# Kernel tuning notes

Hardware: AMD Instinct MI355X
Metric: run time of the kernel (lower is better)

The kernel has to match this reference:

```python
import jax, jax.numpy as jnp
import numpy as np

N = 200000
D_IN = 512
D_OUT = 128

def _xavier(key, shape, gain=1.414):
    fan_in, fan_out = shape
    a = gain * np.sqrt(6.0 / (fan_in + fan_out))
    return jax.random.uniform(key, shape, jnp.float32, -a, a)

def setup_inputs() -> dict:
    key = jax.random.key(0)
    k0, k1, k2, k3 = jax.random.split(key, 4)
    h = jax.random.normal(k0, (N, D_IN), jnp.float32)
    W_Q = _xavier(k1, (D_IN, D_OUT))
    W_K = _xavier(k2, (D_IN, D_OUT))
    W_V = _xavier(k3, (D_IN, D_OUT))
    return {"h": h, "W_Q": W_Q, "W_K": W_K, "W_V": W_V}

def reference(h, W_Q, W_K, W_V):
    # feature maps: elu(x)+1 (positive features for linear attention)
    Q = jax.nn.elu(h @ W_Q) + 1.0          # [N, d]
    K = jax.nn.elu(h @ W_K) + 1.0          # [N, d]
    V = h @ W_V                            # [N, d]
    KV = K.T @ V                           # [d, d] summary
    k_sum = K.sum(axis=0)                  # [d]  (== K.t().sum(dim=1) row-sum per feature)
    Z = 1.0 / (Q @ k_sum[:, None])         # [N, 1]
    out = (Q @ KV) * Z                     # [N, d]
    return jax.nn.elu(out)                 # concat=True -> elu
```

## Files before the change

### kernel.cpp

```cpp
#include <hip/hip_runtime.h>
#include <stdint.h>
#include <stddef.h>


typedef __attribute__((ext_vector_type(8))) short bf16x8;
typedef __attribute__((ext_vector_type(4))) short bf16x4;
typedef __attribute__((ext_vector_type(4))) float f32x4;

#define NROWS   200000
#define DIN     512
#define DOUT    128
#define NCHUNK  3125
#define PA_BLOCKS 512

#define MFMA16(A, B, C) __builtin_amdgcn_mfma_f32_16x16x32_bf16(A, B, C, 0, 0, 0)

__device__ __forceinline__ short f2bf(float f) {
  unsigned u = __builtin_bit_cast(unsigned, f);
  u = (u + 0x7fffu + ((u >> 16) & 1u)) >> 16;
  return (short)u;
}
__device__ __forceinline__ float bf2f(short b) {
  unsigned u = ((unsigned)(unsigned short)b) << 16;
  return __builtin_bit_cast(float, u);
}

__global__ void prep_wt(const float* __restrict__ wq, const float* __restrict__ wk,
                        const float* __restrict__ wv, short* __restrict__ wt) {
  int gid = blockIdx.x * 256 + threadIdx.x;
  int k   = gid >> 5;
  int j4  = (gid & 31) * 4;
  int which = k >> 9;
  int kk    = k & 511;
  const float* W = (which == 0) ? wq : (which == 1) ? wk : wv;
  f32x4 v = *(const f32x4*)(W + (size_t)kk * DOUT + j4);
#pragma unroll
  for (int e = 0; e < 4; ++e)
    wt[(size_t)(which * DOUT + j4 + e) * DIN + kk] = f2bf(v[e]);
}

__global__ __launch_bounds__(512, 2) void pass_a(
    const float* __restrict__ h, const short* __restrict__ wt,
    short* __restrict__ q_ws, float* __restrict__ kv_part,
    float* __restrict__ ksum_part) {
  __shared__ __attribute__((aligned(16))) char smem[32768];
  const int tid = threadIdx.x;
  const int w  = tid >> 6;
  const int l  = tid & 63;
  const int lq = l >> 4;
  const int lr = l & 15;
  const int bid = blockIdx.x;

  const int arow = tid >> 3;
  const int akq  = tid & 7;
  const int sxa  = (arow ^ (arow >> 2)) & 3;
  char* const a_wptr = smem + arow * 64 +
      ((((akq >> 1) ^ sxa) & 3) << 4) + (akq & 1) * 8;

  const int sxl = (lr ^ (lr >> 2)) & 3;
  const char* const a_rbase = smem + lr * 64 + (((lq ^ sxl) & 3) << 4);
  const char* const b_rbase = smem + 4096 + lr * 64 + (((lq ^ sxl) & 3) << 4);

  int b_dst[3], b_src[3];
#pragma unroll
  for (int q = 0; q < 3; ++q) {
    int cc  = q * 512 + tid;
    int col = cc >> 2;
    int sl  = cc & 3;
    int sx  = (col ^ (col >> 2)) & 3;
    b_dst[q] = 4096 + cc * 16;
    b_src[q] = col * DIN + ((sl ^ sx) & 3) * 8;
  }

  const f32x4 zero4 = {0.f, 0.f, 0.f, 0.f};
  f32x4 kvacc[8];
#pragma unroll
  for (int jt = 0; jt < 8; ++jt) kvacc[jt] = zero4;
  float ksum_acc = 0.f;

  for (int c = bid; c < NCHUNK; c += PA_BLOCKS) {
    f32x4 accQ[4], accK[4], accV[4];
#pragma unroll
    for (int rt = 0; rt < 4; ++rt) { accQ[rt] = zero4; accK[rt] = zero4; accV[rt] = zero4; }

    const float* hrow = h + (size_t)(c * 64 + arow) * DIN + akq * 4;
    f32x4  aReg  = *(const f32x4*)(hrow);
    bf16x8 bReg0 = *(const bf16x8*)(wt + b_src[0]);
    bf16x8 bReg1 = *(const bf16x8*)(wt + b_src[1]);
    bf16x8 bReg2 = *(const bf16x8*)(wt + b_src[2]);

    for (int t = 0; t < 16; ++t) {
      __syncthreads();
      bf16x4 a4;
      a4[0] = f2bf(aReg[0]); a4[1] = f2bf(aReg[1]);
      a4[2] = f2bf(aReg[2]); a4[3] = f2bf(aReg[3]);
      *(bf16x4*)a_wptr = a4;
      *(bf16x8*)(smem + b_dst[0]) = bReg0;
      *(bf16x8*)(smem + b_dst[1]) = bReg1;
      *(bf16x8*)(smem + b_dst[2]) = bReg2;
      __syncthreads();
      if (t < 15) {
        aReg  = *(const f32x4*)(hrow + (t + 1) * 32);
        bReg0 = *(const bf16x8*)(wt + b_src[0] + (t + 1) * 32);
        bReg1 = *(const bf16x8*)(wt + b_src[1] + (t + 1) * 32);
        bReg2 = *(const bf16x8*)(wt + b_src[2] + (t + 1) * 32);
      }
      bf16x8 af[4];
#pragma unroll
      for (int rt = 0; rt < 4; ++rt)
        af[rt] = *(const bf16x8*)(a_rbase + rt * 1024);
      bf16x8 bq = *(const bf16x8*)(b_rbase + (w)      * 1024);
      bf16x8 bk = *(const bf16x8*)(b_rbase + (w + 8)  * 1024);
      bf16x8 bv = *(const bf16x8*)(b_rbase + (w + 16) * 1024);
#pragma unroll
      for (int rt = 0; rt < 4; ++rt) {
        accQ[rt] = MFMA16(af[rt], bq, accQ[rt]);
        accK[rt] = MFMA16(af[rt], bk, accK[rt]);
        accV[rt] = MFMA16(af[rt], bv, accV[rt]);
      }
    }

    const int qcol = w * 16 + lr;
    float ks = 0.f;
#pragma unroll
    for (int rt = 0; rt < 4; ++rt) {
      f32x4 qe, ke;
#pragma unroll
      for (int f = 0; f < 4; ++f) {
        float x = accQ[rt][f];
        qe[f] = (x > 0.f) ? (x + 1.f) : __expf(x);
        float y = accK[rt][f];
        ke[f] = (y > 0.f) ? (y + 1.f) : __expf(y);
      }
      short* qp = q_ws + (size_t)(c * 64 + rt * 16 + lq * 4) * DOUT + qcol;
      qp[0]        = f2bf(qe[0]);
      qp[DOUT]     = f2bf(qe[1]);
      qp[2 * DOUT] = f2bf(qe[2]);
      qp[3 * DOUT] = f2bf(qe[3]);
      ks += ke[0] + ke[1] + ke[2] + ke[3];
      bf16x4 kp, vp;
#pragma unroll
      for (int f = 0; f < 4; ++f) { kp[f] = f2bf(ke[f]); vp[f] = f2bf(accV[rt][f]); }
      const int i  = w * 16 + lr;
      const int wb = i * 128 +
          ((((rt * 2 + (lq >> 1)) ^ (lr & 7)) & 7) << 4) + (lq & 1) * 8;
      *(bf16x4*)(smem + wb)          = kp;
      *(bf16x4*)(smem + 16384 + wb)  = vp;
    }
    ks += __shfl_xor(ks, 16);
    ks += __shfl_xor(ks, 32);
    ksum_acc += ks;
    __syncthreads();
#pragma unroll
    for (int ksb = 0; ksb < 2; ++ksb) {
      const int rslot = ((ksb * 4 + lq) ^ (lr & 7)) & 7;
      bf16x8 ka = *(const bf16x8*)(smem + (w * 16 + lr) * 128 + (rslot << 4));
#pragma unroll
      for (int jt = 0; jt < 8; ++jt) {
        bf16x8 vb = *(const bf16x8*)(smem + 16384 + (jt * 16 + lr) * 128 + (rslot << 4));
        kvacc[jt] = MFMA16(ka, vb, kvacc[jt]);
      }
    }
    __syncthreads();
  }

  float* kvp = kv_part + (size_t)bid * 16384;
#pragma unroll
  for (int jt = 0; jt < 8; ++jt)
#pragma unroll
    for (int f = 0; f < 4; ++f)
      kvp[(w * 16 + lq * 4 + f) * 128 + jt * 16 + lr] = kvacc[jt][f];
  if (lq == 0) ksum_part[bid * 128 + w * 16 + lr] = ksum_acc;
}

__global__ void reduce_kv(const float* __restrict__ kv_part,
                          const float* __restrict__ ksum_part,
                          short* __restrict__ kvT, float* __restrict__ ksum) {
  if (blockIdx.x < 128) {
    const int i  = blockIdx.x;
    const int t  = threadIdx.x;
    const int j4 = t & 31;
    const int bs = t >> 5;
    f32x4 acc = {0.f, 0.f, 0.f, 0.f};
#pragma unroll 4
    for (int b = bs * 128; b < bs * 128 + 128; ++b)
      acc += *(const f32x4*)(kv_part + (size_t)b * 16384 + i * 128 + j4 * 4);
    __shared__ f32x4 red[4][32];
    red[bs][j4] = acc;
    __syncthreads();
    if (t < 32) {
      f32x4 s = red[0][t] + red[1][t] + red[2][t] + red[3][t];
#pragma unroll
      for (int e = 0; e < 4; ++e) {
        int j = t * 4 + e;
        kvT[j * 128 + (i ^ ((j & 7) << 3))] = f2bf(s[e]);
      }
    }
  } else {
    const int j = threadIdx.x;
    float s = 0.f;
#pragma unroll 8
    for (int b = 0; b < PA_BLOCKS; ++b) s += ksum_part[b * 128 + j];
    ksum[j] = s;
  }
}

__global__ __launch_bounds__(256, 4) void pass_c(
    const short* __restrict__ q_ws, const short* __restrict__ kvT,
    const float* __restrict__ ksum, float* __restrict__ out) {
  __shared__ __attribute__((aligned(16))) char smem[33024];
  const int tid = threadIdx.x;
  const int w  = tid >> 6, l = tid & 63, lq = l >> 4, lr = l & 15;
  const int rowbase = blockIdx.x * 64 + w * 16;

#pragma unroll
  for (int q = 0; q < 8; ++q) {
    int cc = q * 256 + tid;
    *(bf16x8*)(smem + cc * 16) = *(const bf16x8*)(kvT + cc * 8);
  }

  bf16x8 qa[4];
  float d = 0.f;
  const short* qrow = q_ws + (size_t)(rowbase + lr) * DOUT + lq * 8;
#pragma unroll
  for (int ks = 0; ks < 4; ++ks) {
    qa[ks] = *(const bf16x8*)(qrow + ks * 32);
    f32x4 k0 = *(const f32x4*)(ksum + ks * 32 + lq * 8);
    f32x4 k1 = *(const f32x4*)(ksum + ks * 32 + lq * 8 + 4);
#pragma unroll
    for (int e = 0; e < 4; ++e) d += bf2f(qa[ks][e]) * k0[e];
#pragma unroll
    for (int e = 0; e < 4; ++e) d += bf2f(qa[ks][e + 4]) * k1[e];
  }
  d += __shfl_xor(d, 16);
  d += __shfl_xor(d, 32);
  float* dlds = (float*)(smem + 32768);
  if (l < 16) dlds[w * 16 + lr] = d;
  __syncthreads();

  const f32x4 zero4 = {0.f, 0.f, 0.f, 0.f};
  f32x4 acc[8];
#pragma unroll
  for (int jt = 0; jt < 8; ++jt) acc[jt] = zero4;
#pragma unroll
  for (int ks = 0; ks < 4; ++ks) {
#pragma unroll
    for (int jt = 0; jt < 8; ++jt) {
      const int j    = jt * 16 + lr;
      const int slot = (ks * 4 + lq) ^ (lr & 7);
      bf16x8 bv = *(const bf16x8*)(smem + j * 256 + (slot << 4));
      acc[jt] = MFMA16(qa[ks], bv, acc[jt]);
    }
  }
  float z[4];
#pragma unroll
  for (int f = 0; f < 4; ++f) z[f] = 1.f / dlds[w * 16 + lq * 4 + f];
#pragma unroll
  for (int jt = 0; jt < 8; ++jt) {
#pragma unroll
    for (int f = 0; f < 4; ++f) {
      float v = acc[jt][f] * z[f];
      v = (v > 0.f) ? v : (__expf(v) - 1.f);
      out[(size_t)(rowbase + lq * 4 + f) * DOUT + jt * 16 + lr] = v;
    }
  }
}

extern "C" void kernel_launch(void* const* d_in, const int* in_sizes, int n_in,
                              void* d_out, int out_size, void* d_ws, size_t ws_size,
                              hipStream_t stream) {
  const float* h  = (const float*)d_in[0];
  const float* wq = (const float*)d_in[1];
  const float* wk = (const float*)d_in[2];
  const float* wv = (const float*)d_in[3];
  char* ws = (char*)d_ws;
  short* q_ws      = (short*)(ws);
  short* wt        = (short*)(ws + 51200000);
  float* kv_part   = (float*)(ws + 51593216);
  float* ksum_part = (float*)(ws + 85147648);
  short* kvT       = (short*)(ws + 85409792);
  float* ksum      = (float*)(ws + 85442560);
  float* out       = (float*)d_out;

  prep_wt<<<dim3(192), dim3(256), 0, stream>>>(wq, wk, wv, wt);
  pass_a<<<dim3(PA_BLOCKS), dim3(512), 0, stream>>>(h, wt, q_ws, kv_part, ksum_part);
  reduce_kv<<<dim3(129), dim3(128), 0, stream>>>(kv_part, ksum_part, kvT, ksum);
  pass_c<<<dim3(NCHUNK), dim3(256), 0, stream>>>(q_ws, kvT, ksum, out);
}
```

Before: 838.9 us.

## Split projection into per-weight LDS-resident GEMM tiles with separate KV reduction pass

```diff
diff --git a/kernel.cpp b/kernel.cpp
--- a/kernel.cpp
+++ b/kernel.cpp
@@ -4,14 +4,11 @@
 
 
 typedef __attribute__((ext_vector_type(8))) short bf16x8;
-typedef __attribute__((ext_vector_type(4))) short bf16x4;
 typedef __attribute__((ext_vector_type(4))) float f32x4;
 
 #define NROWS   200000
 #define DIN     512
 #define DOUT    128
-#define NCHUNK  3125
-#define PA_BLOCKS 512
 
 #define MFMA16(A, B, C) __builtin_amdgcn_mfma_f32_16x16x32_bf16(A, B, C, 0, 0, 0)
 
@@ -28,180 +25,203 @@
 __global__ void prep_wt(const float* __restrict__ wq, const float* __restrict__ wk,
                         const float* __restrict__ wv, short* __restrict__ wt) {
   int gid = blockIdx.x * 256 + threadIdx.x;
-  int k   = gid >> 5;
-  int j4  = (gid & 31) * 4;
-  int which = k >> 9;
-  int kk    = k & 511;
-  const float* W = (which == 0) ? wq : (which == 1) ? wk : wv;
-  f32x4 v = *(const f32x4*)(W + (size_t)kk * DOUT + j4);
-#pragma unroll
-  for (int e = 0; e < 4; ++e)
-    wt[(size_t)(which * DOUT + j4 + e) * DIN + kk] = f2bf(v[e]);
-}
-
-__global__ __launch_bounds__(512, 2) void pass_a(
+  int z   = gid >> 13;
+  int col = (gid >> 6) & 127;
+  int s   = gid & 63;
+  const float* W = (z == 0) ? wq : (z == 1) ? wk : wv;
+  bf16x8 o;
+#pragma unroll
+  for (int e = 0; e < 8; ++e)
+    o[e] = f2bf(W[(size_t)(s * 8 + e) * DOUT + col]);
+  *(bf16x8*)((char*)wt + (size_t)z * 131072 + col * 1024 + ((s ^ (col & 7)) * 16)) = o;
+}
+
+__global__ __launch_bounds__(512) void pass_a(
     const float* __restrict__ h, const short* __restrict__ wt,
-    short* __restrict__ q_ws, float* __restrict__ kv_part,
-    float* __restrict__ ksum_part) {
-  __shared__ __attribute__((aligned(16))) char smem[32768];
+    short* __restrict__ q_ws, short* __restrict__ k_ws, short* __restrict__ v_ws) {
+  extern __shared__ __attribute__((aligned(16))) char smem[];
+
+  const int bid  = blockIdx.x;
+  const int xcd  = bid & 7;
+  const int slot = bid >> 3;
+  const int nT   = (xcd < 6) ? 98 : 97;
+  if ((slot / 3) >= nT) return;
+  const int base = (xcd < 6) ? xcd * 98 : 6 * 98 + (xcd - 6) * 97;
+  const int tile = base + slot / 3;
+  const int z    = slot % 3;
+
   const int tid = threadIdx.x;
-  const int w  = tid >> 6;
-  const int l  = tid & 63;
-  const int lq = l >> 4;
-  const int lr = l & 15;
-  const int bid = blockIdx.x;
-
-  const int arow = tid >> 3;
-  const int akq  = tid & 7;
-  const int sxa  = (arow ^ (arow >> 2)) & 3;
-  char* const a_wptr = smem + arow * 64 +
-      ((((akq >> 1) ^ sxa) & 3) << 4) + (akq & 1) * 8;
-
-  const int sxl = (lr ^ (lr >> 2)) & 3;
-  const char* const a_rbase = smem + lr * 64 + (((lq ^ sxl) & 3) << 4);
-  const char* const b_rbase = smem + 4096 + lr * 64 + (((lq ^ sxl) & 3) << 4);
-
-  int b_dst[3], b_src[3];
-#pragma unroll
-  for (int q = 0; q < 3; ++q) {
-    int cc  = q * 512 + tid;
-    int col = cc >> 2;
-    int sl  = cc & 3;
-    int sx  = (col ^ (col >> 2)) & 3;
-    b_dst[q] = 4096 + cc * 16;
-    b_src[q] = col * DIN + ((sl ^ sx) & 3) * 8;
-  }
-
-  const f32x4 zero4 = {0.f, 0.f, 0.f, 0.f};
-  f32x4 kvacc[8];
-#pragma unroll
-  for (int jt = 0; jt < 8; ++jt) kvacc[jt] = zero4;
-  float ksum_acc = 0.f;
-
-  for (int c = bid; c < NCHUNK; c += PA_BLOCKS) {
-    f32x4 accQ[4], accK[4], accV[4];
-#pragma unroll
-    for (int rt = 0; rt < 4; ++rt) { accQ[rt] = zero4; accK[rt] = zero4; accV[rt] = zero4; }
-
-    const float* hrow = h + (size_t)(c * 64 + arow) * DIN + akq * 4;
-    f32x4  aReg  = *(const f32x4*)(hrow);
-    bf16x8 bReg0 = *(const bf16x8*)(wt + b_src[0]);
-    bf16x8 bReg1 = *(const bf16x8*)(wt + b_src[1]);
-    bf16x8 bReg2 = *(const bf16x8*)(wt + b_src[2]);
-
-    for (int t = 0; t < 16; ++t) {
-      __syncthreads();
-      bf16x4 a4;
-      a4[0] = f2bf(aReg[0]); a4[1] = f2bf(aReg[1]);
-      a4[2] = f2bf(aReg[2]); a4[3] = f2bf(aReg[3]);
-      *(bf16x4*)a_wptr = a4;
-      *(bf16x8*)(smem + b_dst[0]) = bReg0;
-      *(bf16x8*)(smem + b_dst[1]) = bReg1;
-      *(bf16x8*)(smem + b_dst[2]) = bReg2;
-      __syncthreads();
-      if (t < 15) {
-        aReg  = *(const f32x4*)(hrow + (t + 1) * 32);
-        bReg0 = *(const bf16x8*)(wt + b_src[0] + (t + 1) * 32);
-        bReg1 = *(const bf16x8*)(wt + b_src[1] + (t + 1) * 32);
-        bReg2 = *(const bf16x8*)(wt + b_src[2] + (t + 1) * 32);
+  const int wv  = tid >> 6;
+  const int l   = tid & 63;
+  const int lr  = l & 15;
+  const int lq  = l >> 4;
+
+  {
+    const char* src = (const char*)wt + (size_t)z * 131072;
+    typedef const __attribute__((address_space(1))) char glb_c;
+    typedef __attribute__((address_space(3))) char lds_c;
+#pragma unroll
+    for (int r = 0; r < 16; ++r) {
+      int off = r * 8192 + (wv * 64) * 16;
+      __builtin_amdgcn_global_load_lds((glb_c*)(src + off + l * 16),
+                                       (lds_c*)(smem + off), 16, 0, 0);
+    }
+  }
+  __syncthreads();
+
+  size_t row0 = (size_t)tile * 256 + wv * 32 + lr;
+  size_t row1 = row0 + 16;
+  size_t r0c = (row0 < NROWS) ? row0 : (size_t)(NROWS - 1);
+  size_t r1c = (row1 < NROWS) ? row1 : (size_t)(NROWS - 1);
+  const float* a0p = h + r0c * DIN + lq * 8;
+  const float* a1p = h + r1c * DIN + lq * 8;
+
+  f32x4 acc[2][8];
+#pragma unroll
+  for (int rt = 0; rt < 2; ++rt)
+#pragma unroll
+    for (int ct = 0; ct < 8; ++ct) acc[rt][ct] = (f32x4){0.f, 0.f, 0.f, 0.f};
+
+  f32x4 c00 = *(const f32x4*)(a0p),     c01 = *(const f32x4*)(a0p + 4);
+  f32x4 c10 = *(const f32x4*)(a1p),     c11 = *(const f32x4*)(a1p + 4);
+
+  for (int ks = 0; ks < 16; ++ks) {
+    f32x4 n00, n01, n10, n11;
+    if (ks < 15) {
+      n00 = *(const f32x4*)(a0p + (ks + 1) * 32);
+      n01 = *(const f32x4*)(a0p + (ks + 1) * 32 + 4);
+      n10 = *(const f32x4*)(a1p + (ks + 1) * 32);
+      n11 = *(const f32x4*)(a1p + (ks + 1) * 32 + 4);
+    }
+    bf16x8 af0, af1;
+#pragma unroll
+    for (int e = 0; e < 4; ++e) {
+      af0[e] = f2bf(c00[e]); af0[e + 4] = f2bf(c01[e]);
+      af1[e] = f2bf(c10[e]); af1[e + 4] = f2bf(c11[e]);
+    }
+#pragma unroll
+    for (int ct = 0; ct < 8; ++ct) {
+      const int col  = ct * 16 + lr;
+      const int s    = (ks * 4 + lq) ^ (l & 7);
+      bf16x8 bf = *(const bf16x8*)(smem + col * 1024 + s * 16);
+      acc[0][ct] = MFMA16(af0, bf, acc[0][ct]);
+      acc[1][ct] = MFMA16(af1, bf, acc[1][ct]);
+    }
+    c00 = n00; c01 = n01; c10 = n10; c11 = n11;
+  }
+
+  short* dst = (z == 0) ? q_ws : (z == 1) ? k_ws : v_ws;
+  const bool isV = (z == 2);
+#pragma unroll
+  for (int rt = 0; rt < 2; ++rt) {
+    size_t rbase = (size_t)tile * 256 + wv * 32 + rt * 16 + lq * 4;
+#pragma unroll
+    for (int ct = 0; ct < 8; ++ct) {
+      const int col = ct * 16 + lr;
+#pragma unroll
+      for (int f = 0; f < 4; ++f) {
+        size_t row = rbase + f;
+        if (row < NROWS) {
+          float x = acc[rt][ct][f];
+          float y = isV ? x : ((x > 0.f) ? (x + 1.f) : __expf(x));
+          dst[row * DOUT + col] = f2bf(y);
+        }
       }
-      bf16x8 af[4];
-#pragma unroll
-      for (int rt = 0; rt < 4; ++rt)
-        af[rt] = *(const bf16x8*)(a_rbase + rt * 1024);
-      bf16x8 bq = *(const bf16x8*)(b_rbase + (w)      * 1024);
-      bf16x8 bk = *(const bf16x8*)(b_rbase + (w + 8)  * 1024);
-      bf16x8 bv = *(const bf16x8*)(b_rbase + (w + 16) * 1024);
-#pragma unroll
-      for (int rt = 0; rt < 4; ++rt) {
-        accQ[rt] = MFMA16(af[rt], bq, accQ[rt]);
-        accK[rt] = MFMA16(af[rt], bk, accK[rt]);
-        accV[rt] = MFMA16(af[rt], bv, accV[rt]);
+    }
+  }
+}
+
+__global__ __launch_bounds__(256) void pass_b(
+    const short* __restrict__ k_ws, const short* __restrict__ v_ws,
+    float* __restrict__ kv_part, float* __restrict__ ksum_part) {
+  __shared__ short KT[128 * 40];
+  __shared__ short VT[128 * 40];
+  __shared__ float kred[32][128];
+
+  const int tid = threadIdx.x;
+  const int w   = tid >> 6;
+  const int l   = tid & 63;
+  const int lr  = l & 15;
+  const int lq  = l >> 4;
+  const int r   = tid >> 3;
+  const int c0  = (tid & 7) * 16;
+
+  f32x4 acc[2][8];
+#pragma unroll
+  for (int rt = 0; rt < 2; ++rt)
+#pragma unroll
+    for (int ct = 0; ct < 8; ++ct) acc[rt][ct] = (f32x4){0.f, 0.f, 0.f, 0.f};
+  float ksa[16];
+#pragma unroll
+  for (int e = 0; e < 16; ++e) ksa[e] = 0.f;
+
+  for (int c = blockIdx.x; c < 6250; c += 256) {
+    size_t rowb = (size_t)c * 32 + r;
+    bf16x8 k0 = *(const bf16x8*)(k_ws + rowb * DOUT + c0);
+    bf16x8 k1 = *(const bf16x8*)(k_ws + rowb * DOUT + c0 + 8);
+    bf16x8 v0 = *(const bf16x8*)(v_ws + rowb * DOUT + c0);
+    bf16x8 v1 = *(const bf16x8*)(v_ws + rowb * DOUT + c0 + 8);
+    __syncthreads();
+#pragma unroll
+    for (int e = 0; e < 8; ++e) {
+      KT[(c0 + e) * 40 + r]     = k0[e];
+      KT[(c0 + 8 + e) * 40 + r] = k1[e];
+      VT[(c0 + e) * 40 + r]     = v0[e];
+      VT[(c0 + 8 + e) * 40 + r] = v1[e];
+      ksa[e]     += bf2f(k0[e]);
+      ksa[e + 8] += bf2f(k1[e]);
+    }
+    __syncthreads();
+    bf16x8 af0 = *(const bf16x8*)(&KT[(w * 32 + lr) * 40 + lq * 8]);
+    bf16x8 af1 = *(const bf16x8*)(&KT[(w * 32 + 16 + lr) * 40 + lq * 8]);
+#pragma unroll
+    for (int ct = 0; ct < 8; ++ct) {
+      bf16x8 bf = *(const bf16x8*)(&VT[(ct * 16 + lr) * 40 + lq * 8]);
+      acc[0][ct] = MFMA16(af0, bf, acc[0][ct]);
+      acc[1][ct] = MFMA16(af1, bf, acc[1][ct]);
+    }
+  }
+
+  float* kvp = kv_part + (size_t)blockIdx.x * 16384;
+#pragma unroll
+  for (int rt = 0; rt < 2; ++rt)
+#pragma unroll
+    for (int ct = 0; ct < 8; ++ct)
+#pragma unroll
+      for (int f = 0; f < 4; ++f) {
+        int i = w * 32 + rt * 16 + lq * 4 + f;
+        int j = ct * 16 + lr;
+        kvp[i * 128 + j] = acc[rt][ct][f];
       }
-    }
-
-    const int qcol = w * 16 + lr;
-    float ks = 0.f;
-#pragma unroll
-    for (int rt = 0; rt < 4; ++rt) {
-      f32x4 qe, ke;
-#pragma unroll
-      for (int f = 0; f < 4; ++f) {
-        float x = accQ[rt][f];
-        qe[f] = (x > 0.f) ? (x + 1.f) : __expf(x);
-        float y = accK[rt][f];
-        ke[f] = (y > 0.f) ? (y + 1.f) : __expf(y);
-      }
-      short* qp = q_ws + (size_t)(c * 64 + rt * 16 + lq * 4) * DOUT + qcol;
-      qp[0]        = f2bf(qe[0]);
-      qp[DOUT]     = f2bf(qe[1]);
-      qp[2 * DOUT] = f2bf(qe[2]);
-      qp[3 * DOUT] = f2bf(qe[3]);
-      ks += ke[0] + ke[1] + ke[2] + ke[3];
-      bf16x4 kp, vp;
-#pragma unroll
-      for (int f = 0; f < 4; ++f) { kp[f] = f2bf(ke[f]); vp[f] = f2bf(accV[rt][f]); }
-      const int i  = w * 16 + lr;
-      const int wb = i * 128 +
-          ((((rt * 2 + (lq >> 1)) ^ (lr & 7)) & 7) << 4) + (lq & 1) * 8;
-      *(bf16x4*)(smem + wb)          = kp;
-      *(bf16x4*)(smem + 16384 + wb)  = vp;
-    }
-    ks += __shfl_xor(ks, 16);
-    ks += __shfl_xor(ks, 32);
-    ksum_acc += ks;
-    __syncthreads();
-#pragma unroll
-    for (int ksb = 0; ksb < 2; ++ksb) {
-      const int rslot = ((ksb * 4 + lq) ^ (lr & 7)) & 7;
-      bf16x8 ka = *(const bf16x8*)(smem + (w * 16 + lr) * 128 + (rslot << 4));
-#pragma unroll
-      for (int jt = 0; jt < 8; ++jt) {
-        bf16x8 vb = *(const bf16x8*)(smem + 16384 + (jt * 16 + lr) * 128 + (rslot << 4));
-        kvacc[jt] = MFMA16(ka, vb, kvacc[jt]);
-      }
-    }
-    __syncthreads();
-  }
-
-  float* kvp = kv_part + (size_t)bid * 16384;
-#pragma unroll
-  for (int jt = 0; jt < 8; ++jt)
-#pragma unroll
-    for (int f = 0; f < 4; ++f)
-      kvp[(w * 16 + lq * 4 + f) * 128 + jt * 16 + lr] = kvacc[jt][f];
-  if (lq == 0) ksum_part[bid * 128 + w * 16 + lr] = ksum_acc;
+  __syncthreads();
+#pragma unroll
+  for (int e = 0; e < 16; ++e) kred[r][c0 + e] = ksa[e];
+  __syncthreads();
+  if (tid < 128) {
+    float s = 0.f;
+#pragma unroll
+    for (int rr = 0; rr < 32; ++rr) s += kred[rr][tid];
+    ksum_part[blockIdx.x * 128 + tid] = s;
+  }
 }
 
 __global__ void reduce_kv(const float* __restrict__ kv_part,
                           const float* __restrict__ ksum_part,
                           short* __restrict__ kvT, float* __restrict__ ksum) {
-  if (blockIdx.x < 128) {
-    const int i  = blockIdx.x;
-    const int t  = threadIdx.x;
-    const int j4 = t & 31;
-    const int bs = t >> 5;
-    f32x4 acc = {0.f, 0.f, 0.f, 0.f};
-#pragma unroll 4
-    for (int b = bs * 128; b < bs * 128 + 128; ++b)
-      acc += *(const f32x4*)(kv_part + (size_t)b * 16384 + i * 128 + j4 * 4);
-    __shared__ f32x4 red[4][32];
-    red[bs][j4] = acc;
-    __syncthreads();
-    if (t < 32) {
-      f32x4 s = red[0][t] + red[1][t] + red[2][t] + red[3][t];
-#pragma unroll
-      for (int e = 0; e < 4; ++e) {
-        int j = t * 4 + e;
-        kvT[j * 128 + (i ^ ((j & 7) << 3))] = f2bf(s[e]);
-      }
-    }
-  } else {
-    const int j = threadIdx.x;
+  if (blockIdx.x < 64) {
+    int e = blockIdx.x * 256 + threadIdx.x;
     float s = 0.f;
 #pragma unroll 8
-    for (int b = 0; b < PA_BLOCKS; ++b) s += ksum_part[b * 128 + j];
-    ksum[j] = s;
+    for (int p = 0; p < 256; ++p) s += kv_part[(size_t)p * 16384 + e];
+    int i = e >> 7, j = e & 127;
+    kvT[j * 128 + (i ^ ((j & 7) << 3))] = f2bf(s);
+  } else {
+    if (threadIdx.x < 128) {
+      float s = 0.f;
+#pragma unroll 8
+      for (int p = 0; p < 256; ++p) s += ksum_part[p * 128 + threadIdx.x];
+      ksum[threadIdx.x] = s;
+    }
   }
 }
 
@@ -238,10 +258,9 @@
   if (l < 16) dlds[w * 16 + lr] = d;
   __syncthreads();
 
-  const f32x4 zero4 = {0.f, 0.f, 0.f, 0.f};
   f32x4 acc[8];
 #pragma unroll
-  for (int jt = 0; jt < 8; ++jt) acc[jt] = zero4;
+  for (int jt = 0; jt < 8; ++jt) acc[jt] = (f32x4){0.f, 0.f, 0.f, 0.f};
 #pragma unroll
   for (int ks = 0; ks < 4; ++ks) {
 #pragma unroll
@@ -275,15 +294,21 @@
   const float* wv = (const float*)d_in[3];
   char* ws = (char*)d_ws;
   short* q_ws      = (short*)(ws);
-  short* wt        = (short*)(ws + 51200000);
-  float* kv_part   = (float*)(ws + 51593216);
-  float* ksum_part = (float*)(ws + 85147648);
-  short* kvT       = (short*)(ws + 85409792);
-  float* ksum      = (float*)(ws + 85442560);
+  short* k_ws      = (short*)(ws + 51200000);
+  short* v_ws      = (short*)(ws + 102400000);
+  short* wt        = (short*)(ws + 153600000);
+  float* kv_part   = (float*)(ws + 153993216);
+  float* ksum_part = (float*)(ws + 170770432);
+  short* kvT       = (short*)(ws + 170901504);
+  float* ksum      = (float*)(ws + 170934272);
   float* out       = (float*)d_out;
 
-  prep_wt<<<dim3(192), dim3(256), 0, stream>>>(wq, wk, wv, wt);
-  pass_a<<<dim3(PA_BLOCKS), dim3(512), 0, stream>>>(h, wt, q_ws, kv_part, ksum_part);
-  reduce_kv<<<dim3(129), dim3(128), 0, stream>>>(kv_part, ksum_part, kvT, ksum);
-  pass_c<<<dim3(NCHUNK), dim3(256), 0, stream>>>(q_ws, kvT, ksum, out);
-}
+  hipFuncSetAttribute((const void*)pass_a,
+                      hipFuncAttributeMaxDynamicSharedMemorySize, 131072);
+
+  prep_wt<<<dim3(96), dim3(256), 0, stream>>>(wq, wk, wv, wt);
+  pass_a<<<dim3(2352), dim3(512), 131072, stream>>>(h, wt, q_ws, k_ws, v_ws);
+  pass_b<<<dim3(256), dim3(256), 0, stream>>>(k_ws, v_ws, kv_part, ksum_part);
+  reduce_kv<<<dim3(65), dim3(256), 0, stream>>>(kv_part, ksum_part, kvT, ksum);
+  pass_c<<<dim3(3125), dim3(256), 0, stream>>>(q_ws, kvT, ksum, out);
+}
```

Result: faster. 748.4 us (-10.8%).
